# Kernel optimization log

Hardware: AMD Instinct MI355X
Metric: run time of the kernel (lower is better)

## Reference

```python
import jax, jax.numpy as jnp
import numpy as np

N, E = 20000, 320000
IN, HID, OUT, EO = 256, 256, 128, 64


def setup_inputs() -> dict:
    key = jax.random.key(0)
    ks = iter(jax.random.split(key, 40))
    w = lambda s: jax.random.normal(next(ks), s, jnp.float32) * 0.05
    inp = {
        "x": jax.random.normal(next(ks), (N, IN), jnp.float32),
        "edge_index": jax.random.randint(next(ks), (2, E), 0, N, jnp.int32),
        "edge_attr": jax.random.uniform(next(ks), (E, 1), jnp.float32),
        # conv1 (IN->IN), conv2 (HID->HID)
        "c1_nw": w((IN, IN)), "c1_ew": w((1, EO)), "c1_new": w((IN + EO, IN)), "c1_b": jnp.zeros((IN,)),
        "c2_nw": w((HID, HID)), "c2_ew": w((1, EO)), "c2_new": w((HID + EO, HID)), "c2_b": jnp.zeros((HID,)),
        # conv3_mean / conv3_logstd (OUT->OUT)
        "cm_nw": w((OUT, OUT)), "cm_ew": w((1, EO)), "cm_new": w((OUT + EO, OUT)), "cm_b": jnp.zeros((OUT,)),
        "cl_nw": w((OUT, OUT)), "cl_ew": w((1, EO)), "cl_new": w((OUT + EO, OUT)), "cl_b": jnp.zeros((OUT,)),
        # linears (stored [in,out])
        "lin1_w": w((IN, HID)), "lin1_b": jnp.zeros((HID,)),
        "lin2_w": w((HID, OUT)), "lin2_b": jnp.zeros((OUT,)),
        "pih_w": w((IN, HID)), "pih_b": jnp.zeros((HID,)),
        "pho_w": w((HID, OUT)), "pho_b": jnp.zeros((OUT,)),
        # batchnorm affine params
        "bn1_g": jnp.ones((IN,)), "bn1_b": jnp.zeros((IN,)),
        "bn2_g": jnp.ones((HID,)), "bn2_b": jnp.zeros((HID,)),
        "bnm_g": jnp.ones((OUT,)), "bnm_b": jnp.zeros((OUT,)),
        "bnl_g": jnp.ones((OUT,)), "bnl_b": jnp.zeros((OUT,)),
    }
    return inp


def _forward(x, edge_index, edge_attr,
             c1_nw, c1_ew, c1_new, c1_b,
             c2_nw, c2_ew, c2_new, c2_b,
             cm_nw, cm_ew, cm_new, cm_b,
             cl_nw, cl_ew, cl_new, cl_b,
             lin1_w, lin1_b, lin2_w, lin2_b,
             pih_w, pih_b, pho_w, pho_b,
             bn1_g, bn1_b, bn2_g, bn2_b,
             bnm_g, bnm_b, bnl_g, bnl_b):
    n = x.shape[0]
    loops = jnp.arange(n, dtype=edge_index.dtype)
    row = jnp.concatenate([edge_index[0], loops])  # source j
    col = jnp.concatenate([edge_index[1], loops])  # target i
    ea = jnp.concatenate([edge_attr, jnp.zeros((n, edge_attr.shape[1]), edge_attr.dtype)], 0)
    deg = jax.ops.segment_sum(jnp.ones_like(col, dtype=x.dtype), col, num_segments=n) + 1e-6
    dis = deg ** -0.5
    norm = dis[row] * dis[col]  # [E+N]

    def gcn(h, nw, ew, new_w, b):
        nm = (h @ nw)[row]                      # gather of x_j @ node_weight
        em = ea @ ew                            # [E+N, EO]
        msg = norm[:, None] * (jnp.concatenate([nm, em], axis=1) @ new_w)
        return jax.ops.segment_sum(msg, col, num_segments=n) + b

    def bn(h, g, b):  # BatchNorm1d, training-mode batch stats, eps 1e-5
        m = h.mean(0)
        v = h.var(0)
        return (h - m) * jax.lax.rsqrt(v + 1e-5) * g + b

    # dropout is identity in eval mode
    x1 = jax.nn.relu(bn(gcn(x, c1_nw, c1_ew, c1_new, c1_b), bn1_g, bn1_b)) + x
    x2 = x1 @ lin1_w + lin1_b
    x2 = jax.nn.relu(bn(gcn(x2, c2_nw, c2_ew, c2_new, c2_b), bn2_g, bn2_b)) + (x1 @ pih_w + pih_b)
    x3 = x2 @ lin2_w + lin2_b
    logstd = bn(gcn(x3, cl_nw, cl_ew, cl_new, cl_b), bnl_g, bnl_b)
    mean = bn(gcn(x3, cm_nw, cm_ew, cm_new, cm_b), bnm_g, bnm_b) + (x2 @ pho_w + pho_b)
    # faithful to source: batch_norm_logstd applied a second time and added
    logstd = logstd + bn(logstd, bnl_g, bnl_b)
    return mean, logstd


def reference(x, edge_index, edge_attr,
              c1_nw, c1_ew, c1_new, c1_b,
              c2_nw, c2_ew, c2_new, c2_b,
              cm_nw, cm_ew, cm_new, cm_b,
              cl_nw, cl_ew, cl_new, cl_b,
              lin1_w, lin1_b, lin2_w, lin2_b,
              pih_w, pih_b, pho_w, pho_b,
              bn1_g, bn1_b, bn2_g, bn2_b,
              bnm_g, bnm_b, bnl_g, bnl_b):
    return _forward(x, edge_index, edge_attr,
                    c1_nw, c1_ew, c1_new, c1_b,
                    c2_nw, c2_ew, c2_new, c2_b,
                    cm_nw, cm_ew, cm_new, cm_b,
                    cl_nw, cl_ew, cl_new, cl_b,
                    lin1_w, lin1_b, lin2_w, lin2_b,
                    pih_w, pih_b, pho_w, pho_b,
                    bn1_g, bn1_b, bn2_g, bn2_b,
                    bnm_g, bnm_b, bnl_g, bnl_b)
```

## Files before the change

### kernel.cpp

```cpp
#include <hip/hip_runtime.h>

#define NN 20000
#define EE 320000
#define ET (EE + NN)

typedef __attribute__((ext_vector_type(8))) short short8v;
typedef __attribute__((ext_vector_type(4))) float float4v;

__device__ __forceinline__ float b2f(unsigned short u) {
  union { float f; unsigned int i; } c; c.i = ((unsigned int)u) << 16; return c.f;
}
__device__ __forceinline__ unsigned short f2bs(float f) {
  union { float f; unsigned int u; } c; c.f = f;
  unsigned int r = c.u + 0x7fffu + ((c.u >> 16) & 1u);
  return (unsigned short)(r >> 16);
}

__global__ void detect_kernel(const unsigned short* __restrict__ x, int* __restrict__ flag) {
  __shared__ int cnt_s;
  if (threadIdx.x == 0) cnt_s = 0;
  __syncthreads();
  int pass = 0;
  for (int j = 0; j < 16; ++j) {
    unsigned short u = x[2 * (threadIdx.x * 16 + j)];
    int e = (u >> 7) & 0xFF;
    if (e >= 96 && e <= 150) pass++;
  }
  atomicAdd(&cnt_s, pass);
  __syncthreads();
  if (threadIdx.x == 0) *flag = (cnt_s < 2458) ? 1 : 0;
}

__global__ void convert_kernel(const void* __restrict__ in, float* __restrict__ out, int n4,
                               const int* __restrict__ flag) {
  int i = blockIdx.x * 256 + threadIdx.x;
  if (i >= n4) return;
  if (*flag) {
    ((float4*)out)[i] = ((const float4*)in)[i];
  } else {
    ushort4 u = ((const ushort4*)in)[i];
    ((float4*)out)[i] = make_float4(b2f(u.x), b2f(u.y), b2f(u.z), b2f(u.w));
  }
}

__global__ void convert_x_kernel(const void* __restrict__ in, float* __restrict__ xc,
                                 short* __restrict__ xh, short* __restrict__ xl, int n4,
                                 const int* __restrict__ flag) {
  int i = blockIdx.x * 256 + threadIdx.x;
  if (i >= n4) return;
  float4 v;
  if (*flag) {
    v = ((const float4*)in)[i];
  } else {
    ushort4 u = ((const ushort4*)in)[i];
    v = make_float4(b2f(u.x), b2f(u.y), b2f(u.z), b2f(u.w));
  }
  ((float4*)xc)[i] = v;
  ushort4 h, l;
  h.x = f2bs(v.x); l.x = f2bs(v.x - b2f(h.x));
  h.y = f2bs(v.y); l.y = f2bs(v.y - b2f(h.y));
  h.z = f2bs(v.z); l.z = f2bs(v.z - b2f(h.z));
  h.w = f2bs(v.w); l.w = f2bs(v.w - b2f(h.w));
  ((ushort4*)xh)[i] = h;
  ((ushort4*)xl)[i] = l;
}

struct WSpec { const void* p[28]; int off[28]; int len[28]; };
__global__ void convert_weights(WSpec ws, float* __restrict__ out, const int* __restrict__ flag) {
  int b = blockIdx.x;
  int f32m = *flag;
  const void* p = ws.p[b];
  int off = ws.off[b], len4 = ws.len[b] >> 2;
  float4* dst = (float4*)(out + off);
  for (int i = blockIdx.y * 256 + threadIdx.x; i < len4; i += 8 * 256) {
    if (f32m) {
      dst[i] = ((const float4*)p)[i];
    } else {
      ushort4 u = ((const ushort4*)p)[i];
      dst[i] = make_float4(b2f(u.x), b2f(u.y), b2f(u.z), b2f(u.w));
    }
  }
}

__global__ void bconv_kernel(const float* __restrict__ W, int ldb,
                             short* __restrict__ Bh, short* __restrict__ Bl, int N) {
  int idx = blockIdx.x * 256 + threadIdx.x;
  if (idx >= N * 256) return;
  int n = idx >> 8, k = idx & 255;
  float v = W[(size_t)k * ldb + n];
  unsigned short h = f2bs(v);
  size_t o = ((size_t)(k >> 3) * N + n) * 8 + (k & 7);
  Bh[o] = (short)h;
  Bl[o] = (short)f2bs(v - b2f(h));
}

__global__ void count_kernel(const int* __restrict__ ei, int* __restrict__ cnt) {
  int e = blockIdx.x * 256 + threadIdx.x;
  if (e >= ET) return;
  int dst = (e < EE) ? ei[EE + e] : (e - EE);
  atomicAdd(&cnt[dst], 1);
}

__global__ void dis_kernel(const int* __restrict__ cnt, float* __restrict__ dis) {
  int i = blockIdx.x * 256 + threadIdx.x;
  if (i >= NN) return;
  dis[i] = rsqrtf((float)cnt[i] + 1e-6f);
}

__global__ void scan1_kernel(const int* __restrict__ cnt, int* __restrict__ partial,
                             int* __restrict__ bsum) {
  __shared__ int sd[256];
  int b = blockIdx.x, t = threadIdx.x;
  int i = b * 256 + t;
  sd[t] = (i < NN) ? cnt[i] : 0;
  __syncthreads();
  for (int off = 1; off < 256; off <<= 1) {
    int x = (t >= off) ? sd[t - off] : 0;
    __syncthreads();
    sd[t] += x;
    __syncthreads();
  }
  if (i < NN) partial[i] = sd[t];
  if (t == 255) bsum[b] = sd[255];
}

__global__ void scan2_kernel(int* __restrict__ bsum, int nb) {
  __shared__ int sd[128];
  int t = threadIdx.x;
  sd[t] = (t < nb) ? bsum[t] : 0;
  __syncthreads();
  for (int off = 1; off < 128; off <<= 1) {
    int x = (t >= off) ? sd[t - off] : 0;
    __syncthreads();
    sd[t] += x;
    __syncthreads();
  }
  if (t < nb) bsum[t] = sd[t];
}

__global__ void scan3_kernel(const int* __restrict__ partial, const int* __restrict__ bsum,
                             int* __restrict__ rowptr) {
  int i = blockIdx.x * 256 + threadIdx.x;
  if (i == 0) rowptr[0] = 0;
  if (i < NN) {
    int b = i >> 8;
    rowptr[i + 1] = partial[i] + (b ? bsum[b - 1] : 0);
  }
}

__global__ void fill_kernel(const int* __restrict__ ei, const float* __restrict__ eaf,
                            const float* __restrict__ dis, const int* __restrict__ rowptr,
                            int* __restrict__ cursor, int* __restrict__ csrc,
                            float* __restrict__ ccoef, float* __restrict__ sarr) {
  int e = blockIdx.x * 256 + threadIdx.x;
  if (e >= ET) return;
  int src, dst; float a;
  if (e < EE) { src = ei[e]; dst = ei[EE + e]; a = eaf[e]; }
  else { src = dst = e - EE; a = 0.f; }
  float coef = dis[src] * dis[dst];
  int pos = rowptr[dst] + atomicAdd(&cursor[dst], 1);
  csrc[pos] = src;
  ccoef[pos] = coef;
  if (a != 0.f) atomicAdd(&sarr[dst], coef * a);
}

struct GJobs {
  const float* A[8]; const float* B[8]; float* C[8];
  int M[8], N[8], K[8], ldc[8], blkx[8], cum[8];
  int njobs;
};
__global__ __launch_bounds__(256) void gemm64_multi(GJobs jb) {
  int bid = blockIdx.x;
  int j = 0;
  while (j < jb.njobs - 1 && bid >= jb.cum[j]) ++j;
  int local = bid - (j ? jb.cum[j - 1] : 0);
  const float* A = jb.A[j];
  const float* B = jb.B[j];
  float* C = jb.C[j];
  int M = jb.M[j], N = jb.N[j], K = jb.K[j], ldc = jb.ldc[j];
  int bx = local % jb.blkx[j], by = local / jb.blkx[j];

  __shared__ float As[16][68];
  __shared__ float Bs[16][64];
  int tid = threadIdx.x;
  int row0 = bx * 64, col0 = by * 64;
  int tr = tid >> 4, tc = tid & 15;
  float acc[4][4] = {};
  int lmA = tid >> 2;
  int lkA = (tid & 3) << 2;
  int lkB = tid >> 4;
  int lcB = (tid & 15) << 2;
  for (int k0 = 0; k0 < K; k0 += 16) {
    int gr = row0 + lmA;
    float4 a4 = make_float4(0.f, 0.f, 0.f, 0.f);
    if (gr < M) a4 = *reinterpret_cast<const float4*>(&A[(size_t)gr * K + k0 + lkA]);
    As[lkA + 0][lmA] = a4.x;
    As[lkA + 1][lmA] = a4.y;
    As[lkA + 2][lmA] = a4.z;
    As[lkA + 3][lmA] = a4.w;
    float4 b4 = *reinterpret_cast<const float4*>(&B[(size_t)(k0 + lkB) * N + col0 + lcB]);
    *reinterpret_cast<float4*>(&Bs[lkB][lcB]) = b4;
    __syncthreads();
#pragma unroll
    for (int kk = 0; kk < 16; ++kk) {
      float4 av = *reinterpret_cast<const float4*>(&As[kk][tr << 2]);
      float4 bv = *reinterpret_cast<const float4*>(&Bs[kk][tc << 2]);
      float aa[4] = {av.x, av.y, av.z, av.w};
      float bb[4] = {bv.x, bv.y, bv.z, bv.w};
#pragma unroll
      for (int i = 0; i < 4; ++i)
#pragma unroll
        for (int jj = 0; jj < 4; ++jj) acc[i][jj] += aa[i] * bb[jj];
    }
    __syncthreads();
  }
#pragma unroll
  for (int i = 0; i < 4; ++i) {
    int gr = row0 + (tr << 2) + i;
    if (gr >= M) continue;
#pragma unroll
    for (int jj = 0; jj < 4; ++jj)
      C[(size_t)gr * ldc + col0 + (tc << 2) + jj] = acc[i][jj];
  }
}

__global__ void copy_strided(const float* __restrict__ src, float* __restrict__ dst,
                             int n, int cshift, int cmask, int ldd) {
  int idx = blockIdx.x * 256 + threadIdx.x;
  if (idx >= n) return;
  int r = idx >> cshift, c = idx & cmask;
  dst[(size_t)r * ldd + c] = src[idx];
}

#define LOADB(ntv, ktv, BH, BL)                                     \
  {                                                                 \
    int n_ = (ntv) * 128 + w * 16 + lm;                             \
    _Pragma("unroll") for (int ks = 0; ks < 2; ++ks) {              \
      int kc = (ktv) * 8 + ks * 4 + lg;                             \
      size_t o = ((size_t)kc * N + n_) * 8;                         \
      BH[ks] = *reinterpret_cast<const short8v*>(Bh + o);           \
      BL[ks] = *reinterpret_cast<const short8v*>(Bl + o);           \
    }                                                               \
  }

__global__ __launch_bounds__(512) void gemm_mfma4(const short* __restrict__ Ah,
                                                  const short* __restrict__ Al,
                                                  const short* __restrict__ Bh,
                                                  const short* __restrict__ Bl,
                                                  unsigned short* __restrict__ C,
                                                  const float* __restrict__ bias,
                                                  int M, int N, int ldc) {
  __shared__ __align__(16) short lds[16384];
  const int K = 256;
  int tid = threadIdx.x;
  int w = tid >> 6, l = tid & 63;
  int row0 = blockIdx.x * 32;
  int lm = l & 15, lg = l >> 4;

#pragma unroll
  for (int i = 0; i < 2; ++i) {
    int id = i * 512 + tid;
    int r = id >> 5, c = id & 31;
    int gr = row0 + r; if (gr >= M) gr = M - 1;
    int sw = c ^ r;
    *reinterpret_cast<float4*>(lds + r * 256 + sw * 8) =
        *reinterpret_cast<const float4*>(Ah + (size_t)gr * K + c * 8);
    *reinterpret_cast<float4*>(lds + 8192 + r * 256 + sw * 8) =
        *reinterpret_cast<const float4*>(Al + (size_t)gr * K + c * 8);
  }
  __syncthreads();

  int NT = N >> 7;
  short8v bhX[2], blX[2], bhY[2], blY[2];
  LOADB(0, 0, bhX, blX);
  for (int nt = 0; nt < NT; ++nt) {
    float4v acc[2] = {};
    int n = nt * 128 + w * 16 + lm;
#pragma unroll
    for (int kt = 0; kt < 4; ++kt) {
      int nt_n = (kt == 3) ? ((nt + 1 < NT) ? nt + 1 : nt) : nt;
      int kt_n = (kt + 1) & 3;
      short8v a_h[2][2], a_l[2][2];
#pragma unroll
      for (int mf = 0; mf < 2; ++mf)
#pragma unroll
        for (int ks = 0; ks < 2; ++ks) {
          int r = mf * 16 + lm;
          int c = kt * 8 + ks * 4 + lg;
          int sw = c ^ r;
          a_h[mf][ks] = *reinterpret_cast<const short8v*>(lds + r * 256 + sw * 8);
          a_l[mf][ks] = *reinterpret_cast<const short8v*>(lds + 8192 + r * 256 + sw * 8);
        }
      if ((kt & 1) == 0) {
        LOADB(nt_n, kt_n, bhY, blY);
#pragma unroll
        for (int mf = 0; mf < 2; ++mf)
#pragma unroll
          for (int ks = 0; ks < 2; ++ks) {
            acc[mf] = __builtin_amdgcn_mfma_f32_16x16x32_bf16(a_h[mf][ks], bhX[ks], acc[mf], 0, 0, 0);
            acc[mf] = __builtin_amdgcn_mfma_f32_16x16x32_bf16(a_h[mf][ks], blX[ks], acc[mf], 0, 0, 0);
            acc[mf] = __builtin_amdgcn_mfma_f32_16x16x32_bf16(a_l[mf][ks], bhX[ks], acc[mf], 0, 0, 0);
          }
      } else {
        LOADB(nt_n, kt_n, bhX, blX);
#pragma unroll
        for (int mf = 0; mf < 2; ++mf)
#pragma unroll
          for (int ks = 0; ks < 2; ++ks) {
            acc[mf] = __builtin_amdgcn_mfma_f32_16x16x32_bf16(a_h[mf][ks], bhY[ks], acc[mf], 0, 0, 0);
            acc[mf] = __builtin_amdgcn_mfma_f32_16x16x32_bf16(a_h[mf][ks], blY[ks], acc[mf], 0, 0, 0);
            acc[mf] = __builtin_amdgcn_mfma_f32_16x16x32_bf16(a_l[mf][ks], bhY[ks], acc[mf], 0, 0, 0);
          }
      }
    }
    float bb = bias ? bias[n] : 0.f;
#pragma unroll
    for (int mf = 0; mf < 2; ++mf)
#pragma unroll
      for (int r = 0; r < 4; ++r) {
        int m = row0 + mf * 16 + lg * 4 + r;
        if (m < M) C[(size_t)m * ldc + n] = f2bs(acc[mf][r] + bb);
      }
  }
}

__global__ void agg_kernel(const unsigned short* __restrict__ U, int ldu,
                           const int* __restrict__ rowptr, const int* __restrict__ csrc,
                           const float* __restrict__ ccoef, const float* __restrict__ sarr,
                           const float* __restrict__ V, float* __restrict__ G) {
  int i = blockIdx.x, t = threadIdx.x;
  float s = sarr[i];
  float4 v4 = ((const float4*)V)[t];
  float ax = s * v4.x, ay = s * v4.y, az = s * v4.z, aw = s * v4.w;
  int p1 = rowptr[i + 1];
  for (int p = rowptr[i]; p < p1; ++p) {
    float c = ccoef[p];
    ushort4 u4 = *reinterpret_cast<const ushort4*>(U + (size_t)csrc[p] * ldu + (t << 2));
    ax += c * b2f(u4.x); ay += c * b2f(u4.y); az += c * b2f(u4.z); aw += c * b2f(u4.w);
  }
  *reinterpret_cast<float4*>(G + (size_t)i * 256 + (t << 2)) = make_float4(ax, ay, az, aw);
}

__global__ void colpart_kernel(const float* __restrict__ h, float* __restrict__ part, int F) {
  __shared__ float4 sm0[256], sm1[256];
  int t = threadIdx.x;
  int cols4 = F >> 2;
  int lc = t & (cols4 - 1);
  int team = t / cols4;
  int rpi = 256 / cols4;
  int r0 = blockIdx.x * 64;
  int r1 = min(r0 + 64, NN);
  float4 s0 = make_float4(0.f, 0.f, 0.f, 0.f);
  float4 s1 = make_float4(0.f, 0.f, 0.f, 0.f);
  for (int r = r0 + team; r < r1; r += rpi) {
    float4 x = *reinterpret_cast<const float4*>(h + (size_t)r * F + lc * 4);
    s0.x += x.x; s0.y += x.y; s0.z += x.z; s0.w += x.w;
    s1.x += x.x * x.x; s1.y += x.y * x.y; s1.z += x.z * x.z; s1.w += x.w * x.w;
  }
  sm0[t] = s0; sm1[t] = s1;
  __syncthreads();
  if (team == 0) {
    for (int k = 1; k < rpi; ++k) {
      float4 a = sm0[k * cols4 + lc];
      float4 b = sm1[k * cols4 + lc];
      s0.x += a.x; s0.y += a.y; s0.z += a.z; s0.w += a.w;
      s1.x += b.x; s1.y += b.y; s1.z += b.z; s1.w += b.w;
    }
    *reinterpret_cast<float4*>(part + (size_t)blockIdx.x * 2 * F + lc * 4) = s0;
    *reinterpret_cast<float4*>(part + (size_t)blockIdx.x * 2 * F + F + lc * 4) = s1;
  }
}

__global__ void bnred_kernel(const float* __restrict__ part, float* __restrict__ part2,
                             int F2, int nb) {
  int c = blockIdx.x * 256 + threadIdx.x;
  if (c >= F2) return;
  int chunk = blockIdx.y;
  int cs = (nb + 7) >> 3;
  int b0 = chunk * cs;
  int b1 = min(b0 + cs, nb);
  float s0 = 0.f, s1 = 0.f, s2 = 0.f, s3 = 0.f;
  int b = b0;
  for (; b + 3 < b1; b += 4) {
    s0 += part[(size_t)(b + 0) * F2 + c];
    s1 += part[(size_t)(b + 1) * F2 + c];
    s2 += part[(size_t)(b + 2) * F2 + c];
    s3 += part[(size_t)(b + 3) * F2 + c];
  }
  for (; b < b1; ++b) s0 += part[(size_t)b * F2 + c];
  part2[(size_t)chunk * F2 + c] = (s0 + s1) + (s2 + s3);
}

__global__ void bnfin_kernel(const float* __restrict__ part2, const float* __restrict__ gamma,
                             const float* __restrict__ beta, int F,
                             float* __restrict__ scsh) {
  int t = threadIdx.x;
  int F2 = 2 * F;
  float s0 = 0.f, s1 = 0.f;
#pragma unroll
  for (int b = 0; b < 8; ++b) {
    s0 += part2[(size_t)b * F2 + t];
    s1 += part2[(size_t)b * F2 + F + t];
  }
  const float invn = 1.f / (float)NN;
  float m = s0 * invn;
  float var = s1 * invn - m * m;
  float sc = gamma[t] * rsqrtf(var + 1e-5f);
  scsh[t] = sc;
  scsh[F + t] = beta[t] - m * sc;
}

__global__ void apply_x1_kernel(const float* __restrict__ g, const float* __restrict__ scsh,
                                const float* __restrict__ xc, short* __restrict__ oh,
                                short* __restrict__ ol, int n) {
  int idx = blockIdx.x * 256 + threadIdx.x;
  if (idx >= n) return;
  int c = idx & 255;
  float y = fmaxf(g[idx] * scsh[c] + scsh[256 + c], 0.f) + xc[idx];
  unsigned short h = f2bs(y);
  oh[idx] = (short)h;
  ol[idx] = (short)f2bs(y - b2f(h));
}

__global__ void apply_x2_kernel(const float* __restrict__ g, const float* __restrict__ scsh,
                                const unsigned short* __restrict__ ucat, short* __restrict__ oh,
                                short* __restrict__ ol, int n) {
  int idx = blockIdx.x * 256 + threadIdx.x;
  if (idx >= n) return;
  int r = idx >> 8, c = idx & 255;
  float y = fmaxf(g[idx] * scsh[c] + scsh[256 + c], 0.f) + b2f(ucat[(size_t)r * 512 + 256 + c]);
  unsigned short h = f2bs(y);
  oh[idx] = (short)h;
  ol[idx] = (short)f2bs(y - b2f(h));
}

__global__ void apply_mean_kernel(const float* __restrict__ g, const float* __restrict__ scsh,
                                  const unsigned short* __restrict__ ucat, float* __restrict__ out,
                                  int n) {
  int idx = blockIdx.x * 256 + threadIdx.x;
  if (idx >= n) return;
  int r = idx >> 7, c = idx & 127;
  float v = g[(size_t)r * 256 + c];
  out[idx] = v * scsh[c] + scsh[256 + c] + b2f(ucat[(size_t)r * 384 + 256 + c]);
}

__global__ void apply_ln0_kernel(const float* __restrict__ g, const float* __restrict__ scsh,
                                 float* __restrict__ L, int n) {
  int idx = blockIdx.x * 256 + threadIdx.x;
  if (idx >= n) return;
  int r = idx >> 7, c = idx & 127;
  float v = g[(size_t)r * 256 + 128 + c];
  L[idx] = v * scsh[128 + c] + scsh[256 + 128 + c];
}

__global__ void apply_ln2_kernel(const float* __restrict__ L, const float* __restrict__ scsh,
                                 float* __restrict__ out, int n) {
  int idx = blockIdx.x * 256 + threadIdx.x;
  if (idx >= n) return;
  int c = idx & 127;
  float v = L[idx];
  out[idx] = v + v * scsh[c] + scsh[128 + c];
}

__global__ void write_code(float* __restrict__ out, float code) {
  int i = blockIdx.x * 256 + threadIdx.x;
  if (i < 4096) out[i] = code;
}

extern "C" void kernel_launch(void* const* d_in, const int* in_sizes, int n_in,
                              void* d_out, int out_size, void* d_ws, size_t ws_size,
                              hipStream_t stream) {
  float* out_mean = (float*)d_out;
  float* out_logstd = out_mean + (size_t)NN * 128;

  static const int expect[35] = {5120000, 640000, 320000,
                                 65536, 64, 81920, 256,  65536, 64, 81920, 256,
                                 16384, 64, 24576, 128,  16384, 64, 24576, 128,
                                 65536, 256, 32768, 128, 65536, 256, 32768, 128,
                                 256, 256, 256, 256, 128, 128, 128, 128};
  if (n_in != 35) { write_code<<<16, 256, 0, stream>>>(out_mean, 900.f); return; }
  if (out_size != 5120000) { write_code<<<16, 256, 0, stream>>>(out_mean, 950.f); return; }
  for (int i = 0; i < 35; ++i)
    if (in_sizes[i] != expect[i]) {
      write_code<<<16, 256, 0, stream>>>(out_mean, 1000.f + 10.f * i);
      return;
    }

  const int* ei = (const int*)d_in[1];

  char* w = (char*)d_ws;
  size_t off = 0;
  auto alloc = [&](size_t bytes) -> void* {
    void* p = w + off;
    off += (bytes + 255) & ~(size_t)255;
    return p;
  };
  int* flag = (int*)alloc(4);
  int* cnt = (int*)alloc(NN * 4);
  int* rowptr = (int*)alloc((NN + 1) * 4);
  int* bsum = (int*)alloc(128 * 4);
  int* csrc = (int*)alloc((size_t)ET * 4);
  float* ccoef = (float*)alloc((size_t)ET * 4);
  float* dis = (float*)alloc(NN * 4);
  float* sarr = (float*)alloc(NN * 4);
  float* eaf = (float*)alloc((size_t)EE * 4);
  float* Wf = (float*)alloc((size_t)576000 * 4);
  float* W1 = (float*)alloc((size_t)65536 * 4);
  float* W2cat = (float*)alloc((size_t)131072 * 4);
  float* W3cat = (float*)alloc((size_t)98304 * 4);
  float* WCa = (float*)alloc((size_t)65536 * 4);
  float* WCb = (float*)alloc((size_t)16384 * 4);
  float* WCc = (float*)alloc((size_t)16384 * 4);
  float* bias2 = (float*)alloc(512 * 4);
  float* bias3 = (float*)alloc(384 * 4);
  float* V1 = (float*)alloc(256 * 4);
  float* V2 = (float*)alloc(256 * 4);
  float* Vcat3 = (float*)alloc(256 * 4);
  float* Gpart = (float*)alloc((size_t)313 * 512 * 4);
  float* Gpart2 = (float*)alloc((size_t)8 * 512 * 4);
  float* scsh = (float*)alloc(512 * 4);
  float* scsh2 = (float*)alloc(256 * 4);
  short* Bh1 = (short*)alloc((size_t)256 * 256 * 2);
  short* Bl1 = (short*)alloc((size_t)256 * 256 * 2);
  short* Bh2 = (short*)alloc((size_t)512 * 256 * 2);
  short* Bl2 = (short*)alloc((size_t)512 * 256 * 2);
  short* Bh3 = (short*)alloc((size_t)384 * 256 * 2);
  short* Bl3 = (short*)alloc((size_t)384 * 256 * 2);
  float* Xc = (float*)alloc((size_t)NN * 256 * 4);
  float* regB = (float*)alloc((size_t)NN * 256 * 4);
  float* regC = (float*)alloc((size_t)NN * 256 * 4);
  float* Ucat = (float*)alloc((size_t)NN * 512 * 4);
  if (off > ws_size) { write_code<<<16, 256, 0, stream>>>(out_mean, 2000.f); return; }

  unsigned short* U1 = (unsigned short*)regB;
  short* X1h = (short*)regB;
  short* X1l = X1h + (size_t)NN * 256;
  short* X2h = X1h;
  short* X2l = X1l;
  short* Xh = (short*)regC;
  short* Xl = Xh + (size_t)NN * 256;
  float* G = regC;
  float* L = Xc;
  unsigned short* Ucat_u = (unsigned short*)Ucat;

  const int n256 = NN * 256, n128 = NN * 128;
  const int g256 = (n256 + 255) / 256, g128 = (n128 + 255) / 256;
  const int nb = (NN + 255) / 256;
  const int nbc = (NN + 63) / 64;

  detect_kernel<<<1, 256, 0, stream>>>((const unsigned short*)d_in[0], flag);
  convert_x_kernel<<<(n256 / 4 + 255) / 256, 256, 0, stream>>>(d_in[0], Xc, Xh, Xl, n256 / 4, flag);
  convert_kernel<<<(EE / 4 + 255) / 256, 256, 0, stream>>>(d_in[2], eaf, EE / 4, flag);

  WSpec wsp;
  const int map[28] = {3, 5, 7, 9, 11, 13, 15, 17, 4, 8, 12, 16, 19, 21, 23, 25,
                       20, 22, 24, 26, 27, 28, 29, 30, 31, 33, 32, 34};
  const int offs[28] = {0, 65536, 147456, 212992, 294912, 311296, 335872, 352256,
                        376832, 376896, 376960, 377024, 377088, 442624, 475392, 540928,
                        573696, 573952, 574080, 574336, 574464, 574720, 574976, 575232,
                        575488, 575616, 575744, 575872};
  const int lens[28] = {65536, 81920, 65536, 81920, 16384, 24576, 16384, 24576,
                        64, 64, 64, 64, 65536, 32768, 65536, 32768,
                        256, 128, 256, 128, 256, 256, 256, 256,
                        128, 128, 128, 128};
  for (int i = 0; i < 28; ++i) { wsp.p[i] = d_in[map[i]]; wsp.off[i] = offs[i]; wsp.len[i] = lens[i]; }
  convert_weights<<<dim3(28, 8), 256, 0, stream>>>(wsp, Wf, flag);

  hipMemsetAsync(cnt, 0, NN * 4, stream);
  count_kernel<<<(ET + 255) / 256, 256, 0, stream>>>(ei, cnt);
  dis_kernel<<<(NN + 255) / 256, 256, 0, stream>>>(cnt, dis);
  scan1_kernel<<<nb, 256, 0, stream>>>(cnt, csrc, bsum);
  scan2_kernel<<<1, 128, 0, stream>>>(bsum, nb);
  scan3_kernel<<<nb, 256, 0, stream>>>(csrc, bsum, rowptr);
  hipMemsetAsync(cnt, 0, NN * 4, stream);
  hipMemsetAsync(sarr, 0, NN * 4, stream);
  fill_kernel<<<(ET + 255) / 256, 256, 0, stream>>>(ei, eaf, dis, rowptr, cnt, csrc, ccoef, sarr);

  {
    GJobs jb{};
    auto set = [&](int j, const float* A, const float* B, float* C, int M, int N, int K,
                   int ldc, int bx, int cum) {
      jb.A[j] = A; jb.B[j] = B; jb.C[j] = C; jb.M[j] = M; jb.N[j] = N; jb.K[j] = K;
      jb.ldc[j] = ldc; jb.blkx[j] = bx; jb.cum[j] = cum;
    };
    set(0, Wf + 0,      Wf + 65536,  W1,          256, 256, 256, 256, 4, 16);
    set(1, Wf + 147456, Wf + 212992, WCa,         256, 256, 256, 256, 4, 32);
    set(2, Wf + 294912, Wf + 311296, WCb,         128, 128, 128, 128, 2, 36);
    set(3, Wf + 335872, Wf + 352256, WCc,         128, 128, 128, 128, 2, 40);
    set(4, Wf + 376832, Wf + 131072, V1,          1,   256, 64,  256, 1, 44);
    set(5, Wf + 376896, Wf + 278528, V2,          1,   256, 64,  256, 1, 48);
    set(6, Wf + 376960, Wf + 327680, Vcat3,       1,   128, 64,  128, 1, 50);
    set(7, Wf + 377024, Wf + 368640, Vcat3 + 128, 1,   128, 64,  128, 1, 52);
    jb.njobs = 8;
    gemm64_multi<<<52, 256, 0, stream>>>(jb);
  }
  {
    GJobs jb{};
    auto set = [&](int j, const float* A, const float* B, float* C, int M, int N, int K,
                   int ldc, int bx, int cum) {
      jb.A[j] = A; jb.B[j] = B; jb.C[j] = C; jb.M[j] = M; jb.N[j] = N; jb.K[j] = K;
      jb.ldc[j] = ldc; jb.blkx[j] = bx; jb.cum[j] = cum;
    };
    set(0, Wf + 377088, WCa, W2cat,       256, 256, 256, 512, 4, 16);
    set(1, Wf + 573696, WCa, bias2,       1,   256, 256, 512, 1, 20);
    set(2, Wf + 442624, WCb, W3cat,       256, 128, 128, 384, 4, 28);
    set(3, Wf + 442624, WCc, W3cat + 128, 256, 128, 128, 384, 4, 36);
    set(4, Wf + 573952, WCb, bias3,       1,   128, 128, 384, 1, 38);
    set(5, Wf + 573952, WCc, bias3 + 128, 1,   128, 128, 384, 1, 40);
    jb.njobs = 6;
    gemm64_multi<<<40, 256, 0, stream>>>(jb);
  }
  copy_strided<<<256, 256, 0, stream>>>(Wf + 475392, W2cat + 256, 65536, 8, 255, 512);
  copy_strided<<<1, 256, 0, stream>>>(Wf + 574080, bias2 + 256, 256, 8, 255, 512);
  copy_strided<<<128, 256, 0, stream>>>(Wf + 540928, W3cat + 256, 32768, 7, 127, 384);
  copy_strided<<<1, 256, 0, stream>>>(Wf + 574336, bias3 + 256, 128, 7, 127, 384);

  bconv_kernel<<<256, 256, 0, stream>>>(W1, 256, Bh1, Bl1, 256);
  bconv_kernel<<<512, 256, 0, stream>>>(W2cat, 512, Bh2, Bl2, 512);
  bconv_kernel<<<384, 256, 0, stream>>>(W3cat, 384, Bh3, Bl3, 384);

  gemm_mfma4<<<625, 512, 0, stream>>>(Xh, Xl, Bh1, Bl1, U1, nullptr, NN, 256, 256);
  agg_kernel<<<NN, 64, 0, stream>>>(U1, 256, rowptr, csrc, ccoef, sarr, V1, G);
  colpart_kernel<<<nbc, 256, 0, stream>>>(G, Gpart, 256);
  bnred_kernel<<<dim3(2, 8), 256, 0, stream>>>(Gpart, Gpart2, 512, nbc);
  bnfin_kernel<<<1, 256, 0, stream>>>(Gpart2, Wf + 574464, Wf + 574720, 256, scsh);
  apply_x1_kernel<<<g256, 256, 0, stream>>>(G, scsh, Xc, X1h, X1l, n256);

  gemm_mfma4<<<625, 512, 0, stream>>>(X1h, X1l, Bh2, Bl2, Ucat_u, bias2, NN, 512, 512);
  agg_kernel<<<NN, 64, 0, stream>>>(Ucat_u, 512, rowptr, csrc, ccoef, sarr, V2, G);
  colpart_kernel<<<nbc, 256, 0, stream>>>(G, Gpart, 256);
  bnred_kernel<<<dim3(2, 8), 256, 0, stream>>>(Gpart, Gpart2, 512, nbc);
  bnfin_kernel<<<1, 256, 0, stream>>>(Gpart2, Wf + 574976, Wf + 575232, 256, scsh);
  apply_x2_kernel<<<g256, 256, 0, stream>>>(G, scsh, Ucat_u, X2h, X2l, n256);

  gemm_mfma4<<<625, 512, 0, stream>>>(X2h, X2l, Bh3, Bl3, Ucat_u, bias3, NN, 384, 384);
  agg_kernel<<<NN, 64, 0, stream>>>(Ucat_u, 384, rowptr, csrc, ccoef, sarr, Vcat3, G);
  colpart_kernel<<<nbc, 256, 0, stream>>>(G, Gpart, 256);
  bnred_kernel<<<dim3(2, 8), 256, 0, stream>>>(Gpart, Gpart2, 512, nbc);
  bnfin_kernel<<<1, 256, 0, stream>>>(Gpart2, Wf + 575488, Wf + 575744, 256, scsh);
  apply_mean_kernel<<<g128, 256, 0, stream>>>(G, scsh, Ucat_u, out_mean, n128);
  apply_ln0_kernel<<<g128, 256, 0, stream>>>(G, scsh, L, n128);
  colpart_kernel<<<nbc, 256, 0, stream>>>(L, Gpart, 128);
  bnred_kernel<<<dim3(1, 8), 256, 0, stream>>>(Gpart, Gpart2, 256, nbc);
  bnfin_kernel<<<1, 128, 0, stream>>>(Gpart2, Wf + 575616, Wf + 575872, 128, scsh2);
  apply_ln2_kernel<<<g128, 256, 0, stream>>>(L, scsh2, out_logstd, n128);
}
```

Measured before the change: 411.5 us.

## Fuse batchnorm column partial sums into aggregation kernel and pack CSR entries

The neighbour aggregation kernel now handles 32 nodes per 256-thread block, four wavefronts each taking nodes in turn. It accumulates per-column sum and sum of squares and writes per-block partials, which removes the separate colpart pass that re-read G three times. CSR source index and coefficient are packed into one int2 array so each edge needs a single 8-byte load. The cost is a larger partial buffer (625 blocks) for bnred to reduce, plus a shared-memory reduction in each block.

```diff
diff --git a/kernel.cpp b/kernel.cpp
--- a/kernel.cpp
+++ b/kernel.cpp
@@ -150,8 +150,8 @@
 
 __global__ void fill_kernel(const int* __restrict__ ei, const float* __restrict__ eaf,
                             const float* __restrict__ dis, const int* __restrict__ rowptr,
-                            int* __restrict__ cursor, int* __restrict__ csrc,
-                            float* __restrict__ ccoef, float* __restrict__ sarr) {
+                            int* __restrict__ cursor, int2* __restrict__ csr,
+                            float* __restrict__ sarr) {
   int e = blockIdx.x * 256 + threadIdx.x;
   if (e >= ET) return;
   int src, dst; float a;
@@ -159,8 +159,7 @@
   else { src = dst = e - EE; a = 0.f; }
   float coef = dis[src] * dis[dst];
   int pos = rowptr[dst] + atomicAdd(&cursor[dst], 1);
-  csrc[pos] = src;
-  ccoef[pos] = coef;
+  csr[pos] = make_int2(src, __float_as_int(coef));
   if (a != 0.f) atomicAdd(&sarr[dst], coef * a);
 }
 
@@ -324,21 +323,47 @@
   }
 }
 
-__global__ void agg_kernel(const unsigned short* __restrict__ U, int ldu,
-                           const int* __restrict__ rowptr, const int* __restrict__ csrc,
-                           const float* __restrict__ ccoef, const float* __restrict__ sarr,
-                           const float* __restrict__ V, float* __restrict__ G) {
-  int i = blockIdx.x, t = threadIdx.x;
-  float s = sarr[i];
+__global__ __launch_bounds__(256) void agg_bn_kernel(const unsigned short* __restrict__ U, int ldu,
+                                                     const int* __restrict__ rowptr,
+                                                     const int2* __restrict__ csr,
+                                                     const float* __restrict__ sarr,
+                                                     const float* __restrict__ V,
+                                                     float* __restrict__ G,
+                                                     float* __restrict__ part) {
+  __shared__ float4 sm0[256], sm1[256];
+  int team = threadIdx.x >> 6;
+  int t = threadIdx.x & 63;
+  int n0 = blockIdx.x * 32;
   float4 v4 = ((const float4*)V)[t];
-  float ax = s * v4.x, ay = s * v4.y, az = s * v4.z, aw = s * v4.w;
-  int p1 = rowptr[i + 1];
-  for (int p = rowptr[i]; p < p1; ++p) {
-    float c = ccoef[p];
-    ushort4 u4 = *reinterpret_cast<const ushort4*>(U + (size_t)csrc[p] * ldu + (t << 2));
-    ax += c * b2f(u4.x); ay += c * b2f(u4.y); az += c * b2f(u4.z); aw += c * b2f(u4.w);
-  }
-  *reinterpret_cast<float4*>(G + (size_t)i * 256 + (t << 2)) = make_float4(ax, ay, az, aw);
+  float4 s0 = make_float4(0.f, 0.f, 0.f, 0.f);
+  float4 s1 = make_float4(0.f, 0.f, 0.f, 0.f);
+  for (int i = n0 + team; i < n0 + 32; i += 4) {
+    float s = sarr[i];
+    float ax = s * v4.x, ay = s * v4.y, az = s * v4.z, aw = s * v4.w;
+    int p1 = rowptr[i + 1];
+    for (int p = rowptr[i]; p < p1; ++p) {
+      int2 e = csr[p];
+      float c = __int_as_float(e.y);
+      ushort4 u4 = *reinterpret_cast<const ushort4*>(U + (size_t)e.x * ldu + (t << 2));
+      ax += c * b2f(u4.x); ay += c * b2f(u4.y); az += c * b2f(u4.z); aw += c * b2f(u4.w);
+    }
+    *reinterpret_cast<float4*>(G + (size_t)i * 256 + (t << 2)) = make_float4(ax, ay, az, aw);
+    s0.x += ax; s0.y += ay; s0.z += az; s0.w += aw;
+    s1.x += ax * ax; s1.y += ay * ay; s1.z += az * az; s1.w += aw * aw;
+  }
+  sm0[threadIdx.x] = s0; sm1[threadIdx.x] = s1;
+  __syncthreads();
+  if (team == 0) {
+#pragma unroll
+    for (int k = 1; k < 4; ++k) {
+      float4 a = sm0[k * 64 + t];
+      float4 b = sm1[k * 64 + t];
+      s0.x += a.x; s0.y += a.y; s0.z += a.z; s0.w += a.w;
+      s1.x += b.x; s1.y += b.y; s1.z += b.z; s1.w += b.w;
+    }
+    *reinterpret_cast<float4*>(part + (size_t)blockIdx.x * 512 + (t << 2)) = s0;
+    *reinterpret_cast<float4*>(part + (size_t)blockIdx.x * 512 + 256 + (t << 2)) = s1;
+  }
 }
 
 __global__ void colpart_kernel(const float* __restrict__ h, float* __restrict__ part, int F) {
@@ -499,8 +524,8 @@
   int* cnt = (int*)alloc(NN * 4);
   int* rowptr = (int*)alloc((NN + 1) * 4);
   int* bsum = (int*)alloc(128 * 4);
-  int* csrc = (int*)alloc((size_t)ET * 4);
-  float* ccoef = (float*)alloc((size_t)ET * 4);
+  int* spart = (int*)alloc(NN * 4);
+  int2* csr = (int2*)alloc((size_t)ET * 8);
   float* dis = (float*)alloc(NN * 4);
   float* sarr = (float*)alloc(NN * 4);
   float* eaf = (float*)alloc((size_t)EE * 4);
@@ -516,7 +541,7 @@
   float* V1 = (float*)alloc(256 * 4);
   float* V2 = (float*)alloc(256 * 4);
   float* Vcat3 = (float*)alloc(256 * 4);
-  float* Gpart = (float*)alloc((size_t)313 * 512 * 4);
+  float* Gpart = (float*)alloc((size_t)625 * 512 * 4);
   float* Gpart2 = (float*)alloc((size_t)8 * 512 * 4);
   float* scsh = (float*)alloc(512 * 4);
   float* scsh2 = (float*)alloc(256 * 4);
@@ -547,6 +572,7 @@
   const int g256 = (n256 + 255) / 256, g128 = (n128 + 255) / 256;
   const int nb = (NN + 255) / 256;
   const int nbc = (NN + 63) / 64;
+  const int nba = 625;
 
   detect_kernel<<<1, 256, 0, stream>>>((const unsigned short*)d_in[0], flag);
   convert_x_kernel<<<(n256 / 4 + 255) / 256, 256, 0, stream>>>(d_in[0], Xc, Xh, Xl, n256 / 4, flag);
@@ -569,12 +595,12 @@
   hipMemsetAsync(cnt, 0, NN * 4, stream);
   count_kernel<<<(ET + 255) / 256, 256, 0, stream>>>(ei, cnt);
   dis_kernel<<<(NN + 255) / 256, 256, 0, stream>>>(cnt, dis);
-  scan1_kernel<<<nb, 256, 0, stream>>>(cnt, csrc, bsum);
+  scan1_kernel<<<nb, 256, 0, stream>>>(cnt, spart, bsum);
   scan2_kernel<<<1, 128, 0, stream>>>(bsum, nb);
-  scan3_kernel<<<nb, 256, 0, stream>>>(csrc, bsum, rowptr);
+  scan3_kernel<<<nb, 256, 0, stream>>>(spart, bsum, rowptr);
   hipMemsetAsync(cnt, 0, NN * 4, stream);
   hipMemsetAsync(sarr, 0, NN * 4, stream);
-  fill_kernel<<<(ET + 255) / 256, 256, 0, stream>>>(ei, eaf, dis, rowptr, cnt, csrc, ccoef, sarr);
+  fill_kernel<<<(ET + 255) / 256, 256, 0, stream>>>(ei, eaf, dis, rowptr, cnt, csr, sarr);
 
   {
     GJobs jb{};
@@ -620,23 +646,20 @@
   bconv_kernel<<<384, 256, 0, stream>>>(W3cat, 384, Bh3, Bl3, 384);
 
   gemm_mfma4<<<625, 512, 0, stream>>>(Xh, Xl, Bh1, Bl1, U1, nullptr, NN, 256, 256);
-  agg_kernel<<<NN, 64, 0, stream>>>(U1, 256, rowptr, csrc, ccoef, sarr, V1, G);
-  colpart_kernel<<<nbc, 256, 0, stream>>>(G, Gpart, 256);
-  bnred_kernel<<<dim3(2, 8), 256, 0, stream>>>(Gpart, Gpart2, 512, nbc);
+  agg_bn_kernel<<<nba, 256, 0, stream>>>(U1, 256, rowptr, csr, sarr, V1, G, Gpart);
+  bnred_kernel<<<dim3(2, 8), 256, 0, stream>>>(Gpart, Gpart2, 512, nba);
   bnfin_kernel<<<1, 256, 0, stream>>>(Gpart2, Wf + 574464, Wf + 574720, 256, scsh);
   apply_x1_kernel<<<g256, 256, 0, stream>>>(G, scsh, Xc, X1h, X1l, n256);
 
   gemm_mfma4<<<625, 512, 0, stream>>>(X1h, X1l, Bh2, Bl2, Ucat_u, bias2, NN, 512, 512);
-  agg_kernel<<<NN, 64, 0, stream>>>(Ucat_u, 512, rowptr, csrc, ccoef, sarr, V2, G);
-  colpart_kernel<<<nbc, 256, 0, stream>>>(G, Gpart, 256);
-  bnred_kernel<<<dim3(2, 8), 256, 0, stream>>>(Gpart, Gpart2, 512, nbc);
+  agg_bn_kernel<<<nba, 256, 0, stream>>>(Ucat_u, 512, rowptr, csr, sarr, V2, G, Gpart);
+  bnred_kernel<<<dim3(2, 8), 256, 0, stream>>>(Gpart, Gpart2, 512, nba);
   bnfin_kernel<<<1, 256, 0, stream>>>(Gpart2, Wf + 574976, Wf + 575232, 256, scsh);
   apply_x2_kernel<<<g256, 256, 0, stream>>>(G, scsh, Ucat_u, X2h, X2l, n256);
 
   gemm_mfma4<<<625, 512, 0, stream>>>(X2h, X2l, Bh3, Bl3, Ucat_u, bias3, NN, 384, 384);
-  agg_kernel<<<NN, 64, 0, stream>>>(Ucat_u, 384, rowptr, csrc, ccoef, sarr, Vcat3, G);
-  colpart_kernel<<<nbc, 256, 0, stream>>>(G, Gpart, 256);
-  bnred_kernel<<<dim3(2, 8), 256, 0, stream>>>(Gpart, Gpart2, 512, nbc);
+  agg_bn_kernel<<<nba, 256, 0, stream>>>(Ucat_u, 384, rowptr, csr, sarr, Vcat3, G, Gpart);
+  bnred_kernel<<<dim3(2, 8), 256, 0, stream>>>(Gpart, Gpart2, 512, nba);
   bnfin_kernel<<<1, 256, 0, stream>>>(Gpart2, Wf + 575488, Wf + 575744, 256, scsh);
   apply_mean_kernel<<<g128, 256, 0, stream>>>(G, scsh, Ucat_u, out_mean, n128);
   apply_ln0_kernel<<<g128, 256, 0, stream>>>(G, scsh, L, n128);
```

New measurement: 576.2 us. 1.4x slower.
